# Kernel optimization log

Measured on AMD Instinct MI355X. Metric: run time of the kernel, lower is better.

## Reference

```python
import jax, jax.numpy as jnp
import numpy as np

B, D_IN, N_CLASSES, N_NODES, D_2D = 512, 512, 16, 100000, 2
EPS = 1e-8  # torch cosine_similarity eps


def setup_inputs() -> dict:
    key = jax.random.key(0)
    k0, k1, k2, k3, k4 = jax.random.split(key, 5)
    logits = jax.random.normal(k0, (B, N_CLASSES), dtype=jnp.float32)
    train_data = jax.random.normal(k1, (B, D_IN), dtype=jnp.float32)
    all_nodes = jax.random.normal(k2, (N_NODES, N_CLASSES), dtype=jnp.float32)
    all_nodes_2d = jax.random.normal(k3, (N_NODES, D_2D), dtype=jnp.float32)
    W = jax.random.normal(k4, (D_IN, D_2D), dtype=jnp.float32) * 0.02
    b = jnp.zeros((D_2D,), dtype=jnp.float32)
    return {"logits": logits, "train_data": train_data, "all_nodes": all_nodes,
            "all_nodes_2d": all_nodes_2d, "W": W, "b": b}


def reference(logits, train_data, all_nodes, all_nodes_2d, W, b):
    # model(train_data): linear 512 -> 2 projection
    emb = train_data @ W + b                                  # (B, 2)
    probs = jax.nn.softmax(logits, axis=1)                    # (B, C)
    pred_class = jnp.argmax(probs, axis=1)                    # (B,)
    node_class = jnp.argmax(all_nodes, axis=1)                # (N,)

    # cosine similarity between each sample's probs and every node (B, N)
    p_norm = jnp.linalg.norm(probs, axis=1, keepdims=True)    # (B, 1)
    n_norm = jnp.linalg.norm(all_nodes, axis=1)               # (N,)
    sim = (probs @ all_nodes.T) / jnp.maximum(p_norm * n_norm[None, :], EPS)

    # masked nearest-neighbor search: only nodes whose argmax class matches
    # the sample's predicted class are candidates (equivalent to the per-sample
    # boolean filtering + argmax in the original loop; first-match tie-break).
    masked_sim = jnp.where(pred_class[:, None] == node_class[None, :], sim, -jnp.inf)
    closest = jnp.argmax(masked_sim, axis=1)                  # (B,)

    target = all_nodes_2d[closest]                            # (B, 2)
    per_sample_mse = jnp.mean((emb - target) ** 2, axis=1)    # (B,)
    return jnp.mean(per_sample_mse)                           # scalar
```

## Files before the change

kernel.cpp:

```cpp
#include <hip/hip_runtime.h>

#define BATCH 512
#define DIN 512
#define NCLS 16
#define NNODES 100000

#define WS_BEST   0
#define WS_PROBS  4096
#define WS_EMB    36864
#define WS_BCNT   40960
#define WS_BLST   41024

__device__ __forceinline__ unsigned ford(float f) {
    unsigned bits = __float_as_uint(f);
    return (bits & 0x80000000u) ? ~bits : (bits | 0x80000000u);
}

__global__ __launch_bounds__(64) void prep_kernel(
    const float* __restrict__ logits,
    const float* __restrict__ train_data,
    const float* __restrict__ W,
    const float* __restrict__ bvec,
    float* __restrict__ probs,
    float* __restrict__ emb,
    int* __restrict__ bucket_count,
    int* __restrict__ bucket_list,
    unsigned long long* __restrict__ best) {
    const int s = blockIdx.x;
    const int lane = threadIdx.x;

    float acc0 = 0.f, acc1 = 0.f;
    const float* td = train_data + s * DIN;
    const float2* W2 = (const float2*)W;
    for (int k = lane; k < DIN; k += 64) {
        float t = td[k];
        float2 w = W2[k];
        acc0 += t * w.x;
        acc1 += t * w.y;
    }
    for (int off = 32; off; off >>= 1) {
        acc0 += __shfl_down(acc0, off);
        acc1 += __shfl_down(acc1, off);
    }

    if (lane == 0) {
        emb[2 * s]     = acc0 + bvec[0];
        emb[2 * s + 1] = acc1 + bvec[1];

        float l[NCLS];
        float m = -1e30f;
        int pred = 0;
        for (int j = 0; j < NCLS; ++j) {
            l[j] = logits[s * NCLS + j];
            if (l[j] > m) { m = l[j]; pred = j; }
        }
        float sum = 0.f;
        for (int j = 0; j < NCLS; ++j) { l[j] = expf(l[j] - m); sum += l[j]; }
        float inv = 1.0f / sum;
        for (int j = 0; j < NCLS; ++j) probs[s * NCLS + j] = l[j] * inv;

        int pos = atomicAdd(&bucket_count[pred], 1);
        bucket_list[pred * BATCH + pos] = s;
        best[s] = 0ull;
    }
}

__global__ __launch_bounds__(256) void nodes_kernel(
    const float* __restrict__ all_nodes,
    const float* __restrict__ probs,
    const int* __restrict__ bucket_count,
    const int* __restrict__ bucket_list,
    unsigned long long* __restrict__ best) {
    __shared__ float sprobs[BATCH * NCLS];
    __shared__ int scount[NCLS];
    __shared__ unsigned long long lbest[BATCH];

    const int t = threadIdx.x;

    for (int i = t; i < BATCH * NCLS / 4; i += 256)
        ((float4*)sprobs)[i] = ((const float4*)probs)[i];
    if (t < NCLS) scount[t] = bucket_count[t];
    for (int i = t; i < BATCH; i += 256) lbest[i] = 0ull;
    __syncthreads();

    const int n = blockIdx.x * 256 + t;
    if (n < NNODES) {
        const float4* nv = (const float4*)(all_nodes + n * NCLS);
        float4 v0 = nv[0], v1 = nv[1], v2 = nv[2], v3 = nv[3];
        float vals[NCLS] = {v0.x, v0.y, v0.z, v0.w, v1.x, v1.y, v1.z, v1.w,
                            v2.x, v2.y, v2.z, v2.w, v3.x, v3.y, v3.z, v3.w};
        int cls = 0;
        float m = vals[0];
        float nrm2 = 0.f;
        #pragma unroll
        for (int j = 0; j < NCLS; ++j) {
            if (j > 0 && vals[j] > m) { m = vals[j]; cls = j; }
            nrm2 += vals[j] * vals[j];
        }
        float inv_norm = 1.0f / sqrtf(nrm2);

        const int cnt = scount[cls];
        const int* lst = bucket_list + cls * BATCH;
        for (int i = 0; i < cnt; ++i) {
            int s = lst[i];
            const float4* p4 = (const float4*)(sprobs + s * NCLS);
            float4 a0 = p4[0], a1 = p4[1], a2 = p4[2], a3 = p4[3];
            float dot = a0.x * v0.x + a0.y * v0.y + a0.z * v0.z + a0.w * v0.w
                      + a1.x * v1.x + a1.y * v1.y + a1.z * v1.z + a1.w * v1.w
                      + a2.x * v2.x + a2.y * v2.y + a2.z * v2.z + a2.w * v2.w
                      + a3.x * v3.x + a3.y * v3.y + a3.z * v3.z + a3.w * v3.w;
            float sim = dot * inv_norm;
            unsigned long long packed =
                ((unsigned long long)ford(sim) << 32) | (unsigned long long)(0xFFFFFFFFu - (unsigned)n);
            atomicMax(&lbest[s], packed);
        }
    }
    __syncthreads();
    for (int i = t; i < BATCH; i += 256)
        if (lbest[i]) atomicMax(&best[i], lbest[i]);
}

__global__ __launch_bounds__(512) void finalize_kernel(
    const unsigned long long* __restrict__ best,
    const float* __restrict__ emb,
    const float* __restrict__ all_nodes_2d,
    float* __restrict__ out) {
    const int s = threadIdx.x;
    unsigned long long p = best[s];
    int idx = (p == 0ull) ? 0 : (int)(0xFFFFFFFFu - (unsigned)(p & 0xFFFFFFFFull));
    float t0 = all_nodes_2d[2 * idx];
    float t1 = all_nodes_2d[2 * idx + 1];
    float d0 = emb[2 * s] - t0;
    float d1 = emb[2 * s + 1] - t1;
    float v = 0.5f * (d0 * d0 + d1 * d1);

    for (int off = 32; off; off >>= 1) v += __shfl_down(v, off);
    __shared__ float partial[8];
    if ((s & 63) == 0) partial[s >> 6] = v;
    __syncthreads();
    if (s == 0) {
        float sum = 0.f;
        for (int i = 0; i < 8; ++i) sum += partial[i];
        out[0] = sum / (float)BATCH;
    }
}

extern "C" void kernel_launch(void* const* d_in, const int* in_sizes, int n_in,
                              void* d_out, int out_size, void* d_ws, size_t ws_size,
                              hipStream_t stream) {
    const float* logits       = (const float*)d_in[0];
    const float* train_data   = (const float*)d_in[1];
    const float* all_nodes    = (const float*)d_in[2];
    const float* all_nodes_2d = (const float*)d_in[3];
    const float* W            = (const float*)d_in[4];
    const float* bvec         = (const float*)d_in[5];
    float* out = (float*)d_out;

    char* ws = (char*)d_ws;
    unsigned long long* best = (unsigned long long*)(ws + WS_BEST);
    float* probs             = (float*)(ws + WS_PROBS);
    float* emb               = (float*)(ws + WS_EMB);
    int* bucket_count        = (int*)(ws + WS_BCNT);
    int* bucket_list         = (int*)(ws + WS_BLST);

    hipMemsetAsync(bucket_count, 0, NCLS * sizeof(int), stream);

    prep_kernel<<<BATCH, 64, 0, stream>>>(logits, train_data, W, bvec,
                                          probs, emb, bucket_count, bucket_list, best);

    int nblocks = (NNODES + 255) / 256;
    nodes_kernel<<<nblocks, 256, 0, stream>>>(all_nodes, probs, bucket_count,
                                              bucket_list, best);

    finalize_kernel<<<1, BATCH, 0, stream>>>(best, emb, all_nodes_2d, out);
}
```

Baseline: 100.1 us.

## Fuse finalize into nodes kernel, drop memset, restructure prep and shared layout

Removes the memset and the separate finalize launch. The last nodes block, found with an atomic done counter, now computes the MSE. Prep becomes 65 blocks: 64 compute embeddings with 8 waves each, and one block runs softmax and a counting sort of samples by class through shared atomics, writing class offsets. The nodes kernel copies the sorted ids into shared memory, stores probs in a transposed float4 layout, and skips the LDS atomicMax when the packed value cannot win. Fewer launches and less atomic traffic are traded for a single-block sort and a threadfence/last-block pattern.

```diff
diff --git a/kernel.cpp b/kernel.cpp
--- a/kernel.cpp
+++ b/kernel.cpp
@@ -4,86 +4,125 @@
 #define DIN 512
 #define NCLS 16
 #define NNODES 100000
+#define CBLK 256
+#define NODE_BLOCKS ((NNODES + CBLK - 1) / CBLK)
 
 #define WS_BEST   0
 #define WS_PROBS  4096
 #define WS_EMB    36864
-#define WS_BCNT   40960
-#define WS_BLST   41024
+#define WS_SORT   40960
+#define WS_OFF    43008
+#define WS_DONE   43136
 
 __device__ __forceinline__ unsigned ford(float f) {
     unsigned bits = __float_as_uint(f);
     return (bits & 0x80000000u) ? ~bits : (bits | 0x80000000u);
 }
 
-__global__ __launch_bounds__(64) void prep_kernel(
+__global__ __launch_bounds__(512) void prep_kernel(
     const float* __restrict__ logits,
     const float* __restrict__ train_data,
     const float* __restrict__ W,
     const float* __restrict__ bvec,
     float* __restrict__ probs,
     float* __restrict__ emb,
-    int* __restrict__ bucket_count,
-    int* __restrict__ bucket_list,
-    unsigned long long* __restrict__ best) {
-    const int s = blockIdx.x;
-    const int lane = threadIdx.x;
-
-    float acc0 = 0.f, acc1 = 0.f;
-    const float* td = train_data + s * DIN;
-    const float2* W2 = (const float2*)W;
-    for (int k = lane; k < DIN; k += 64) {
-        float t = td[k];
-        float2 w = W2[k];
-        acc0 += t * w.x;
-        acc1 += t * w.y;
-    }
-    for (int off = 32; off; off >>= 1) {
-        acc0 += __shfl_down(acc0, off);
-        acc1 += __shfl_down(acc1, off);
-    }
-
-    if (lane == 0) {
-        emb[2 * s]     = acc0 + bvec[0];
-        emb[2 * s + 1] = acc1 + bvec[1];
-
-        float l[NCLS];
-        float m = -1e30f;
+    int* __restrict__ sorted_ids,
+    int* __restrict__ class_off,
+    unsigned long long* __restrict__ best,
+    unsigned int* __restrict__ done) {
+    if (blockIdx.x < 64) {
+        const int wave = threadIdx.x >> 6;
+        const int lane = threadIdx.x & 63;
+        const int s = blockIdx.x * 8 + wave;
+        const float* td = train_data + s * DIN;
+        const float2* W2 = (const float2*)W;
+        float a0 = 0.f, a1 = 0.f;
+        for (int k = lane; k < DIN; k += 64) {
+            float t = td[k];
+            float2 w = W2[k];
+            a0 += t * w.x;
+            a1 += t * w.y;
+        }
+        for (int off = 32; off; off >>= 1) {
+            a0 += __shfl_down(a0, off);
+            a1 += __shfl_down(a1, off);
+        }
+        if (lane == 0) {
+            emb[2 * s]     = a0 + bvec[0];
+            emb[2 * s + 1] = a1 + bvec[1];
+        }
+    } else {
+        __shared__ int scnt[NCLS];
+        __shared__ int soff[NCLS + 1];
+        const int s = threadIdx.x;
+        if (s < NCLS) scnt[s] = 0;
+
+        const float4* lg = (const float4*)(logits + s * NCLS);
+        float4 x0 = lg[0], x1 = lg[1], x2 = lg[2], x3 = lg[3];
+        float v[NCLS] = {x0.x, x0.y, x0.z, x0.w, x1.x, x1.y, x1.z, x1.w,
+                         x2.x, x2.y, x2.z, x2.w, x3.x, x3.y, x3.z, x3.w};
+        float m = v[0];
         int pred = 0;
-        for (int j = 0; j < NCLS; ++j) {
-            l[j] = logits[s * NCLS + j];
-            if (l[j] > m) { m = l[j]; pred = j; }
-        }
+        #pragma unroll
+        for (int j = 1; j < NCLS; ++j)
+            if (v[j] > m) { m = v[j]; pred = j; }
         float sum = 0.f;
-        for (int j = 0; j < NCLS; ++j) { l[j] = expf(l[j] - m); sum += l[j]; }
+        #pragma unroll
+        for (int j = 0; j < NCLS; ++j) { v[j] = expf(v[j] - m); sum += v[j]; }
         float inv = 1.0f / sum;
-        for (int j = 0; j < NCLS; ++j) probs[s * NCLS + j] = l[j] * inv;
-
-        int pos = atomicAdd(&bucket_count[pred], 1);
-        bucket_list[pred * BATCH + pos] = s;
+        float4* p4 = (float4*)(probs + s * NCLS);
+        p4[0] = make_float4(v[0] * inv, v[1] * inv, v[2] * inv, v[3] * inv);
+        p4[1] = make_float4(v[4] * inv, v[5] * inv, v[6] * inv, v[7] * inv);
+        p4[2] = make_float4(v[8] * inv, v[9] * inv, v[10] * inv, v[11] * inv);
+        p4[3] = make_float4(v[12] * inv, v[13] * inv, v[14] * inv, v[15] * inv);
+
         best[s] = 0ull;
+
+        __syncthreads();
+        int pos = atomicAdd(&scnt[pred], 1);
+        __syncthreads();
+        if (s == 0) {
+            int acc = 0;
+            for (int c = 0; c < NCLS; ++c) { soff[c] = acc; acc += scnt[c]; }
+            soff[NCLS] = acc;
+            *done = 0u;
+        }
+        __syncthreads();
+        sorted_ids[soff[pred] + pos] = s;
+        if (s <= NCLS) class_off[s] = soff[s];
     }
 }
 
 __global__ __launch_bounds__(256) void nodes_kernel(
     const float* __restrict__ all_nodes,
     const float* __restrict__ probs,
-    const int* __restrict__ bucket_count,
-    const int* __restrict__ bucket_list,
-    unsigned long long* __restrict__ best) {
-    __shared__ float sprobs[BATCH * NCLS];
-    __shared__ int scount[NCLS];
+    const int* __restrict__ sorted_ids,
+    const int* __restrict__ class_off,
+    unsigned long long* __restrict__ best,
+    unsigned int* __restrict__ done,
+    const float* __restrict__ emb,
+    const float* __restrict__ all_nodes_2d,
+    float* __restrict__ out) {
+    __shared__ float4 sp4[4 * BATCH];
     __shared__ unsigned long long lbest[BATCH];
+    __shared__ int ssort[BATCH];
+    __shared__ int soff[NCLS + 1];
+    __shared__ int slast;
+    __shared__ float part[4];
 
     const int t = threadIdx.x;
 
-    for (int i = t; i < BATCH * NCLS / 4; i += 256)
-        ((float4*)sprobs)[i] = ((const float4*)probs)[i];
-    if (t < NCLS) scount[t] = bucket_count[t];
-    for (int i = t; i < BATCH; i += 256) lbest[i] = 0ull;
-    __syncthreads();
-
-    const int n = blockIdx.x * 256 + t;
+    const float4* p4 = (const float4*)probs;
+    for (int i = t; i < 4 * BATCH; i += CBLK)
+        sp4[(i & 3) * BATCH + (i >> 2)] = p4[i];
+    for (int i = t; i < BATCH; i += CBLK) {
+        lbest[i] = 0ull;
+        ssort[i] = sorted_ids[i];
+    }
+    if (t <= NCLS) soff[t] = class_off[t];
+    __syncthreads();
+
+    const int n = blockIdx.x * CBLK + t;
     if (n < NNODES) {
         const float4* nv = (const float4*)(all_nodes + n * NCLS);
         float4 v0 = nv[0], v1 = nv[1], v2 = nv[2], v3 = nv[3];
@@ -98,50 +137,52 @@
             nrm2 += vals[j] * vals[j];
         }
         float inv_norm = 1.0f / sqrtf(nrm2);
-
-        const int cnt = scount[cls];
-        const int* lst = bucket_list + cls * BATCH;
-        for (int i = 0; i < cnt; ++i) {
-            int s = lst[i];
-            const float4* p4 = (const float4*)(sprobs + s * NCLS);
-            float4 a0 = p4[0], a1 = p4[1], a2 = p4[2], a3 = p4[3];
+        unsigned low = 0xFFFFFFFFu - (unsigned)n;
+
+        const int i0 = soff[cls], i1 = soff[cls + 1];
+        for (int i = i0; i < i1; ++i) {
+            int s = ssort[i];
+            float4 a0 = sp4[s];
+            float4 a1 = sp4[BATCH + s];
+            float4 a2 = sp4[2 * BATCH + s];
+            float4 a3 = sp4[3 * BATCH + s];
             float dot = a0.x * v0.x + a0.y * v0.y + a0.z * v0.z + a0.w * v0.w
                       + a1.x * v1.x + a1.y * v1.y + a1.z * v1.z + a1.w * v1.w
                       + a2.x * v2.x + a2.y * v2.y + a2.z * v2.z + a2.w * v2.w
                       + a3.x * v3.x + a3.y * v3.y + a3.z * v3.z + a3.w * v3.w;
             float sim = dot * inv_norm;
             unsigned long long packed =
-                ((unsigned long long)ford(sim) << 32) | (unsigned long long)(0xFFFFFFFFu - (unsigned)n);
-            atomicMax(&lbest[s], packed);
-        }
-    }
-    __syncthreads();
-    for (int i = t; i < BATCH; i += 256)
-        if (lbest[i]) atomicMax(&best[i], lbest[i]);
-}
-
-__global__ __launch_bounds__(512) void finalize_kernel(
-    const unsigned long long* __restrict__ best,
-    const float* __restrict__ emb,
-    const float* __restrict__ all_nodes_2d,
-    float* __restrict__ out) {
-    const int s = threadIdx.x;
-    unsigned long long p = best[s];
-    int idx = (p == 0ull) ? 0 : (int)(0xFFFFFFFFu - (unsigned)(p & 0xFFFFFFFFull));
-    float t0 = all_nodes_2d[2 * idx];
-    float t1 = all_nodes_2d[2 * idx + 1];
-    float d0 = emb[2 * s] - t0;
-    float d1 = emb[2 * s + 1] - t1;
-    float v = 0.5f * (d0 * d0 + d1 * d1);
-
-    for (int off = 32; off; off >>= 1) v += __shfl_down(v, off);
-    __shared__ float partial[8];
-    if ((s & 63) == 0) partial[s >> 6] = v;
-    __syncthreads();
-    if (s == 0) {
-        float sum = 0.f;
-        for (int i = 0; i < 8; ++i) sum += partial[i];
-        out[0] = sum / (float)BATCH;
+                ((unsigned long long)ford(sim) << 32) | (unsigned long long)low;
+            if (packed > lbest[s]) atomicMax(&lbest[s], packed);
+        }
+    }
+    __syncthreads();
+    for (int i = t; i < BATCH; i += CBLK) {
+        unsigned long long b = lbest[i];
+        if (b) atomicMax(&best[i], b);
+    }
+    __threadfence();
+    __syncthreads();
+    if (t == 0)
+        slast = (atomicAdd(done, 1u) == (unsigned)(gridDim.x - 1)) ? 1 : 0;
+    __syncthreads();
+    if (slast) {
+        float v = 0.f;
+        for (int i = t; i < BATCH; i += CBLK) {
+            unsigned long long p = atomicMax(&best[i], 0ull);
+            int idx = (p == 0ull) ? 0
+                                  : (int)(0xFFFFFFFFu - (unsigned)(p & 0xFFFFFFFFull));
+            float2 tgt = ((const float2*)all_nodes_2d)[idx];
+            float2 e = ((const float2*)emb)[i];
+            float d0 = e.x - tgt.x;
+            float d1 = e.y - tgt.y;
+            v += 0.5f * (d0 * d0 + d1 * d1);
+        }
+        for (int off = 32; off; off >>= 1) v += __shfl_down(v, off);
+        if ((t & 63) == 0) part[t >> 6] = v;
+        __syncthreads();
+        if (t == 0)
+            out[0] = (part[0] + part[1] + part[2] + part[3]) / (float)BATCH;
     }
 }
 
@@ -160,17 +201,16 @@
     unsigned long long* best = (unsigned long long*)(ws + WS_BEST);
     float* probs             = (float*)(ws + WS_PROBS);
     float* emb               = (float*)(ws + WS_EMB);
-    int* bucket_count        = (int*)(ws + WS_BCNT);
-    int* bucket_list         = (int*)(ws + WS_BLST);
-
-    hipMemsetAsync(bucket_count, 0, NCLS * sizeof(int), stream);
-
-    prep_kernel<<<BATCH, 64, 0, stream>>>(logits, train_data, W, bvec,
-                                          probs, emb, bucket_count, bucket_list, best);
-
-    int nblocks = (NNODES + 255) / 256;
-    nodes_kernel<<<nblocks, 256, 0, stream>>>(all_nodes, probs, bucket_count,
-                                              bucket_list, best);
-
-    finalize_kernel<<<1, BATCH, 0, stream>>>(best, emb, all_nodes_2d, out);
-}
+    int* sorted_ids          = (int*)(ws + WS_SORT);
+    int* class_off           = (int*)(ws + WS_OFF);
+    unsigned int* done       = (unsigned int*)(ws + WS_DONE);
+
+    prep_kernel<<<65, 512, 0, stream>>>(logits, train_data, W, bvec,
+                                        probs, emb, sorted_ids, class_off,
+                                        best, done);
+
+    nodes_kernel<<<NODE_BLOCKS, CBLK, 0, stream>>>(all_nodes, probs,
+                                                   sorted_ids, class_off,
+                                                   best, done,
+                                                   emb, all_nodes_2d, out);
+}
```

Measured after the change: 107.4 us. 7.3% more time.
